# Kernel tuning notes

Hardware: AMD Instinct MI355X
Metric: run time of the kernel (lower is better)

The kernel has to match this reference:

```python
import jax, jax.numpy as jnp
import numpy as np

IOU_TH = 0.5      # iou_threshold
SCORE_TH = 0.5    # confidence_threshold (passed as score_threshold to tf NMS)
MAX_DET = 512     # max_detections


def setup_inputs() -> dict:
    key = jax.random.key(0)
    k1, k2, k3 = jax.random.split(key, 3)
    B, N, C = 8, 2048, 80
    # tf.image.non_max_suppression interprets box columns as corners
    # (y1, x1, y2, x2); generate valid corner boxes in [0, 1].
    mins = jax.random.uniform(k1, (B, N, 2), dtype=jnp.float32)
    sizes = jax.random.uniform(k2, (B, N, 2), dtype=jnp.float32) * 0.2 + 0.01
    box_prediction = jnp.concatenate([mins, mins + sizes], axis=-1)  # [B,N,4]
    class_prediction = jax.random.normal(k3, (B, N, C), dtype=jnp.float32) * 2.0
    return {"box_prediction": box_prediction, "class_prediction": class_prediction}


def _nms_single(boxes, cls_pred, conf):
    """Greedy NMS for one image. boxes [N,4], cls_pred [N,C], conf [N].
    Matches tf.image.non_max_suppression semantics (corner-coordinate IoU,
    score threshold, greedy suppression in descending score order),
    then gathers boxes/cls/conf at the kept indices, padded to MAX_DET."""
    N = boxes.shape[0]
    order = jnp.argsort(-conf)                 # descending scores
    b = boxes[order]                            # [N,4]
    c = cls_pred[order]                         # [N,C]
    s = conf[order]                             # [N]

    bb = jax.lax.stop_gradient(b)               # IoU/indices are non-diff
    y1, x1, y2, x2 = bb[:, 0], bb[:, 1], bb[:, 2], bb[:, 3]
    area = (y2 - y1) * (x2 - x1)                # [N]
    ih = jnp.clip(jnp.minimum(y2[:, None], y2[None, :]) -
                  jnp.maximum(y1[:, None], y1[None, :]), 0.0)
    iw = jnp.clip(jnp.minimum(x2[:, None], x2[None, :]) -
                  jnp.maximum(x1[:, None], x1[None, :]), 0.0)
    inter = ih * iw                             # [N,N]
    union = area[:, None] + area[None, :] - inter
    iou = inter / jnp.maximum(union, 1e-9)      # [N,N]

    valid = s > SCORE_TH                        # score_threshold filter
    idxs = jnp.arange(N)

    def step(keep, xs):
        row, i = xs
        # if box i survives, suppress all later boxes overlapping > IOU_TH
        sup = (row > IOU_TH) & (idxs > i) & keep[i]
        return keep & ~sup, None

    keep, _ = jax.lax.scan(step, valid, (iou, idxs))

    # select kept boxes (already sorted by score) padded to MAX_DET
    masked = jnp.where(keep, s, -1.0)
    top_s, top_idx = jax.lax.top_k(jax.lax.stop_gradient(masked), MAX_DET)
    vm = top_s > SCORE_TH                       # validity of each output slot
    out_box = b[top_idx] * vm[:, None].astype(b.dtype)
    out_cls = c[top_idx] * vm[:, None].astype(c.dtype)
    out_conf = jnp.where(vm, s[top_idx], 0.0)
    return out_box, out_cls, out_conf


def reference(box_prediction, class_prediction):
    # from_logits=True branch of the layer
    class_confidence = jnp.max(jax.nn.sigmoid(class_prediction), axis=-1)  # [B,N]
    cls_prob = jax.nn.softmax(class_prediction, axis=-1)                   # [B,N,C]
    nms_box, nms_cls, nms_conf = jax.vmap(_nms_single)(
        box_prediction, cls_prob, class_confidence)
    return nms_box, nms_cls, nms_conf
```

## Files before the change

### kernel.cpp

```cpp
#include <hip/hip_runtime.h>
#include <stdint.h>

#define BB 8
#define NN 2048
#define NC 80
#define MAXDET 512
#define WPR 32


#define ORD_HALF 0xBF000000u

__global__ __launch_bounds__(64) void k_conf(const float* __restrict__ cls,
                                             uint64_t* __restrict__ keys) {
    int gid = blockIdx.x * 64 + threadIdx.x;
    const float4* p = (const float4*)(cls + (size_t)gid * NC);
    float m = -3.0e38f;
#pragma unroll
    for (int i = 0; i < NC / 4; ++i) {
        float4 v = p[i];
        m = fmaxf(m, fmaxf(fmaxf(v.x, v.y), fmaxf(v.z, v.w)));
    }
    float e  = expf(-m);
    float cf = 1.0f / (1.0f + e);
    uint32_t u = __float_as_uint(cf);
    u = (u & 0x80000000u) ? ~u : (u | 0x80000000u);
    int n = gid & (NN - 1);
    keys[gid] = ((uint64_t)u << 32) | (uint32_t)(NN - 1 - n);
}

#define RCHUNK 128
__global__ __launch_bounds__(512) void k_rank(const uint64_t* __restrict__ keys_in,
                                              uint64_t* __restrict__ keys_out,
                                              const float* __restrict__ boxes,
                                              float* __restrict__ sboxes) {
    __shared__ uint64_t sk[NN];
    __shared__ uint16_t part[4][RCHUNK];
    int b = blockIdx.y, t = threadIdx.x;
    const uint64_t* kin = keys_in + (size_t)b * NN;
#pragma unroll
    for (int j = 0; j < NN / 512; ++j)
        sk[t + j * 512] = kin[t + j * 512];
    __syncthreads();
    int sub = t >> 7;
    int el  = t & (RCHUNK - 1);
    int e   = blockIdx.x * RCHUNK + el;
    uint64_t mykey = sk[e];
    int base = sub * (NN / 4);
    int r = 0;
    for (int mm = 0; mm < NN / 4; ++mm)
        r += (sk[base + mm] > mykey) ? 1 : 0;
    part[sub][el] = (uint16_t)r;
    __syncthreads();
    if (t < RCHUNK) {
        int rank = part[0][t] + part[1][t] + part[2][t] + part[3][t];
        keys_out[(size_t)b * NN + rank] = mykey;
        int orig = (NN - 1) - (int)(mykey & 0xFFFFFFFFull);
        ((float4*)sboxes)[(size_t)b * NN + rank] =
            ((const float4*)boxes)[(size_t)b * NN + orig];
    }
}

__global__ void k_sup(const float* __restrict__ sboxes, uint64_t* __restrict__ sup) {
#pragma clang fp contract(off)
    __shared__ float cy1[256], cx1[256], cy2[256], cx2[256], car[256];
    __shared__ float ry1[64], rx1[64], ry2[64], rx2[64], rar[64];
    int rt = blockIdx.x, ct = blockIdx.y, b = blockIdx.z;
    int t = threadIdx.x;
    int col0 = ct << 8, row0 = rt << 6;
    {
        float4 bx = ((const float4*)sboxes)[(size_t)b * NN + col0 + t];
        cy1[t] = bx.x; cx1[t] = bx.y; cy2[t] = bx.z; cx2[t] = bx.w;
        car[t] = (bx.z - bx.x) * (bx.w - bx.y);
        if (t < 64) {
            float4 rb = ((const float4*)sboxes)[(size_t)b * NN + row0 + t];
            ry1[t] = rb.x; rx1[t] = rb.y; ry2[t] = rb.z; rx2[t] = rb.w;
            rar[t] = (rb.z - rb.x) * (rb.w - rb.y);
        }
    }
    __syncthreads();
    int lr = t & 63, lg = t >> 6;
    int r = row0 + lr;
    int gw = (ct << 2) + lg;
    int cbase = gw << 6;
    uint64_t w = 0;
    if (cbase + 63 > r) {
        float y1 = ry1[lr], x1 = rx1[lr], y2 = ry2[lr], x2 = rx2[lr], ar = rar[lr];
        int lcb = lg << 6;
        for (int c = 0; c < 64; ++c) {
            int lc = lcb + c;
            float ih = fmaxf(fminf(y2, cy2[lc]) - fmaxf(y1, cy1[lc]), 0.0f);
            float iw = fmaxf(fminf(x2, cx2[lc]) - fmaxf(x1, cx1[lc]), 0.0f);
            float inter = ih * iw;
            float uni = (ar + car[lc]) - inter;
            float iou = inter / fmaxf(uni, 1e-9f);
            if ((iou > 0.5f) & ((cbase + c) > r)) w |= (1ull << c);
        }
    }
    sup[((size_t)b * NN + r) * WPR + gw] = w;
}

#define NMS_THREADS 320
__global__ __launch_bounds__(NMS_THREADS) void k_nms(const uint64_t* __restrict__ keys,
                                                     const float* __restrict__ sboxes,
                                                     const uint64_t* __restrict__ sup,
                                                     int* __restrict__ kidx,
                                                     int* __restrict__ kcount,
                                                     float* __restrict__ out_box,
                                                     float* __restrict__ out_conf) {
    __shared__ uint64_t buf[2][64 * WPR];
    __shared__ uint64_t dgT[2][64];
    __shared__ uint8_t  val[NN];
    __shared__ uint64_t kmaskS[WPR];
    __shared__ int pfx[WPR];
    __shared__ int s_kc;
    __shared__ int s_done;
    int b = blockIdx.x, t = threadIdx.x;
    const uint64_t* supb = sup + (size_t)b * NN * WPR;
    const uint64_t* keyb = keys + (size_t)b * NN;

    for (int i = t; i < NN; i += NMS_THREADS)
        val[i] = (uint8_t)((uint32_t)(keyb[i] >> 32) > ORD_HALF);
    if (t < WPR) kmaskS[t] = 0;
    if (t == 0) s_done = 0;
    for (int e = t; e < 64 * WPR / 2; e += NMS_THREADS) {
        ulonglong2 v = ((const ulonglong2*)supb)[e];
        ((ulonglong2*)buf[0])[e] = v;
        if ((e & 15) == 0) dgT[0][e >> 4] = v.x;
    }
    __syncthreads();

    int wave = t >> 6;
    uint64_t kb = 0;
    int cnt = 0;
    if (t < 32) {
        uint64_t vm = 0;
#pragma unroll
        for (int c = 0; c < 64; ++c)
            vm |= ((uint64_t)val[(t << 6) | c]) << c;
        kb = ~vm;
    }
    int l2 = t & 31, half = (t >> 5) & 1;

    for (int g = 0; g < WPR; ++g) {
        if (wave > 0) {
            if (g + 1 < WPR) {
                const ulonglong2* src = (const ulonglong2*)(supb + (size_t)(g + 1) * 64 * WPR);
                ulonglong2* dst = (ulonglong2*)buf[(g + 1) & 1];
                int idx = t - 64;
                ulonglong2 r0 = src[idx];
                ulonglong2 r1 = src[idx + 256];
                ulonglong2 r2 = src[idx + 512];
                ulonglong2 r3 = src[idx + 768];
                dst[idx]       = r0;
                dst[idx + 256] = r1;
                dst[idx + 512] = r2;
                dst[idx + 768] = r3;
                if ((idx & 15) == ((g + 1) >> 1)) {
                    int r = idx >> 4;
                    int hi = (g + 1) & 1;
                    uint64_t* dT = dgT[(g + 1) & 1];
                    dT[r]      = hi ? r0.y : r0.x;
                    dT[r + 16] = hi ? r1.y : r1.x;
                    dT[r + 32] = hi ? r2.y : r2.x;
                    dT[r + 48] = hi ? r3.y : r3.x;
                }
            }
        } else {
            const uint64_t* bufc = buf[g & 1];
            uint64_t diag = dgT[g & 1][t];
            uint32_t dlo = (uint32_t)diag, dhi = (uint32_t)(diag >> 32);
            uint64_t rwv = __shfl(kb, g);
            uint32_t rw_lo = __builtin_amdgcn_readfirstlane((uint32_t)rwv);
            uint32_t rw_hi = __builtin_amdgcn_readfirstlane((uint32_t)(rwv >> 32));
            uint32_t gm_lo = 0, gm_hi = 0;
#pragma unroll
            for (int c = 0; c < 32; ++c) {
                uint32_t rlo = __builtin_amdgcn_readlane(dlo, c);
                uint32_t rhi = __builtin_amdgcn_readlane(dhi, c);
                uint32_t keep = (~(rw_lo >> c)) & 1u;
                uint32_t msk  = 0u - keep;
                rw_lo |= rlo & msk;
                rw_hi |= rhi & msk;
                gm_lo |= keep << c;
            }
#pragma unroll
            for (int c = 0; c < 32; ++c) {
                uint32_t rlo = __builtin_amdgcn_readlane(dlo, c + 32);
                uint32_t rhi = __builtin_amdgcn_readlane(dhi, c + 32);
                uint32_t keep = (~(rw_hi >> c)) & 1u;
                uint32_t msk  = 0u - keep;
                rw_lo |= rlo & msk;
                rw_hi |= rhi & msk;
                gm_hi |= keep << c;
            }
            uint64_t gm = ((uint64_t)gm_hi << 32) | gm_lo;
            uint32_t gmh = half ? gm_hi : gm_lo;
            const uint64_t* rowp = bufc + ((half << 5) * WPR + l2);
            uint64_t acc = 0;
#pragma unroll
            for (int j = 0; j < 32; ++j) {
                uint64_t row = rowp[(size_t)j * WPR];
                acc |= (((gmh >> j) & 1u) ? row : 0ull);
            }
            acc |= __shfl(acc, t ^ 32);
            if (t < 32) kb |= acc;
            if (t == g) kmaskS[g] = gm;
            cnt += __popcll(gm);
            if (cnt >= MAXDET) s_done = 1;
        }
        __syncthreads();
        if (s_done) break;
    }

    if (t == 0) {
        int s = 0;
        for (int w2 = 0; w2 < WPR; ++w2) { pfx[w2] = s; s += __popcll(kmaskS[w2]); }
        s_kc = (s < MAXDET) ? s : MAXDET;
        kcount[b] = s_kc;
    }
    __syncthreads();
    for (int i = t; i < NN; i += NMS_THREADS) {
        uint64_t m = kmaskS[i >> 6];
        if ((m >> (i & 63)) & 1ull) {
            int rank = pfx[i >> 6] + __popcll(m & ((1ull << (i & 63)) - 1ull));
            if (rank < MAXDET) {
                ((float4*)out_box)[(size_t)b * MAXDET + rank] =
                    ((const float4*)sboxes)[(size_t)b * NN + i];
                uint64_t kk = keyb[i];
                uint32_t u = (uint32_t)(kk >> 32);
                float cf = (u & 0x80000000u) ? __uint_as_float(u ^ 0x80000000u)
                                             : __uint_as_float(~u);
                out_conf[(size_t)b * MAXDET + rank] = cf;
                kidx[b * MAXDET + rank] = (NN - 1) - (int)(kk & 0xFFFFFFFFull);
            }
        }
    }
    for (int k = s_kc + t; k < MAXDET; k += NMS_THREADS) {
        ((float4*)out_box)[(size_t)b * MAXDET + k] = make_float4(0.f, 0.f, 0.f, 0.f);
        out_conf[(size_t)b * MAXDET + k] = 0.0f;
    }
}

__global__ void k_softmax(const float* __restrict__ cls, const int* __restrict__ kidx,
                          const int* __restrict__ kcount, float* __restrict__ out_cls) {
    int k = blockIdx.x, b = blockIdx.y, lane = threadIdx.x;
    float* dst = out_cls + ((size_t)b * MAXDET + k) * NC;
    if (k >= kcount[b]) {
        dst[lane] = 0.0f;
        if (lane < NC - 64) dst[64 + lane] = 0.0f;
        return;
    }
    int n = kidx[b * MAXDET + k];
    const float* src = cls + ((size_t)b * NN + n) * NC;
    float x0 = src[lane];
    float x1 = (lane < NC - 64) ? src[64 + lane] : -3.0e38f;
    float m = fmaxf(x0, x1);
    for (int o = 32; o > 0; o >>= 1) m = fmaxf(m, __shfl_xor(m, o));
    float e0 = expf(x0 - m);
    float e1 = (lane < NC - 64) ? expf(x1 - m) : 0.0f;
    float s = e0 + e1;
    for (int o = 32; o > 0; o >>= 1) s += __shfl_xor(s, o);
    dst[lane] = e0 / s;
    if (lane < NC - 64) dst[64 + lane] = e1 / s;
}

extern "C" void kernel_launch(void* const* d_in, const int* in_sizes, int n_in,
                              void* d_out, int out_size, void* d_ws, size_t ws_size,
                              hipStream_t stream) {
    const float* boxes = (const float*)d_in[0];
    const float* cls   = (const float*)d_in[1];
    float* out      = (float*)d_out;
    float* out_box  = out;
    float* out_cls  = out + BB * MAXDET * 4;
    float* out_conf = out + BB * MAXDET * (4 + NC);

    char* ws = (char*)d_ws;
    uint64_t* keysA  = (uint64_t*)(ws + 0);
    uint64_t* keysB  = (uint64_t*)(ws + 131072);
    float*    sboxes = (float*)(ws + 262144);
    int*      kidx   = (int*)(ws + 524288);
    int*      kcount = (int*)(ws + 540672);
    uint64_t* sup    = (uint64_t*)(ws + 544768);

    k_conf<<<(BB * NN) / 64, 64, 0, stream>>>(cls, keysA);
    k_rank<<<dim3(NN / RCHUNK, BB), 512, 0, stream>>>(keysA, keysB, boxes, sboxes);
    k_sup<<<dim3(NN / 64, NN / 256, BB), 256, 0, stream>>>(sboxes, sup);
    k_nms<<<BB, NMS_THREADS, 0, stream>>>(keysB, sboxes, sup, kidx, kcount, out_box, out_conf);
    k_softmax<<<dim3(MAXDET, BB), 64, 0, stream>>>(cls, kidx, kcount, out_cls);
}
```

Before: 80.19 us.

## Prefetch suppression rows two groups ahead with register staging and triple buffer

The NMS kernel's loader waves now issue global loads for group g+2 into registers, while the registers already holding group g+1 are written into a triple-buffered shared array. This hides global-load latency behind a whole iteration instead of stalling on it before the LDS store each step. The cost is extra LDS (a third 16KB buffer plus diagonal slot) and more live registers in the loader waves.

```diff
diff --git a/kernel.cpp b/kernel.cpp
--- a/kernel.cpp
+++ b/kernel.cpp
@@ -107,8 +107,8 @@
                                                      int* __restrict__ kcount,
                                                      float* __restrict__ out_box,
                                                      float* __restrict__ out_conf) {
-    __shared__ uint64_t buf[2][64 * WPR];
-    __shared__ uint64_t dgT[2][64];
+    __shared__ uint64_t buf[3][64 * WPR];
+    __shared__ uint64_t dgT[3][64];
     __shared__ uint8_t  val[NN];
     __shared__ uint64_t kmaskS[WPR];
     __shared__ int pfx[WPR];
@@ -127,9 +127,16 @@
         ((ulonglong2*)buf[0])[e] = v;
         if ((e & 15) == 0) dgT[0][e >> 4] = v.x;
     }
-    __syncthreads();
 
     int wave = t >> 6;
+    int idx = t - 64;
+    ulonglong2 s0 = {}, s1 = {}, s2 = {}, s3 = {};
+    if (wave > 0) {
+        const ulonglong2* src = (const ulonglong2*)(supb + (size_t)64 * WPR);
+        s0 = src[idx]; s1 = src[idx + 256]; s2 = src[idx + 512]; s3 = src[idx + 768];
+    }
+    __syncthreads();
+
     uint64_t kb = 0;
     int cnt = 0;
     if (t < 32) {
@@ -141,33 +148,33 @@
     }
     int l2 = t & 31, half = (t >> 5) & 1;
 
+    int rd = 0;
     for (int g = 0; g < WPR; ++g) {
+        int wr = (rd == 2) ? 0 : rd + 1;
         if (wave > 0) {
             if (g + 1 < WPR) {
-                const ulonglong2* src = (const ulonglong2*)(supb + (size_t)(g + 1) * 64 * WPR);
-                ulonglong2* dst = (ulonglong2*)buf[(g + 1) & 1];
-                int idx = t - 64;
-                ulonglong2 r0 = src[idx];
-                ulonglong2 r1 = src[idx + 256];
-                ulonglong2 r2 = src[idx + 512];
-                ulonglong2 r3 = src[idx + 768];
-                dst[idx]       = r0;
-                dst[idx + 256] = r1;
-                dst[idx + 512] = r2;
-                dst[idx + 768] = r3;
+                ulonglong2* dst = (ulonglong2*)buf[wr];
+                dst[idx]       = s0;
+                dst[idx + 256] = s1;
+                dst[idx + 512] = s2;
+                dst[idx + 768] = s3;
                 if ((idx & 15) == ((g + 1) >> 1)) {
                     int r = idx >> 4;
                     int hi = (g + 1) & 1;
-                    uint64_t* dT = dgT[(g + 1) & 1];
-                    dT[r]      = hi ? r0.y : r0.x;
-                    dT[r + 16] = hi ? r1.y : r1.x;
-                    dT[r + 32] = hi ? r2.y : r2.x;
-                    dT[r + 48] = hi ? r3.y : r3.x;
+                    uint64_t* dT = dgT[wr];
+                    dT[r]      = hi ? s0.y : s0.x;
+                    dT[r + 16] = hi ? s1.y : s1.x;
+                    dT[r + 32] = hi ? s2.y : s2.x;
+                    dT[r + 48] = hi ? s3.y : s3.x;
                 }
             }
+            if (g + 2 < WPR) {
+                const ulonglong2* src = (const ulonglong2*)(supb + (size_t)(g + 2) * 64 * WPR);
+                s0 = src[idx]; s1 = src[idx + 256]; s2 = src[idx + 512]; s3 = src[idx + 768];
+            }
         } else {
-            const uint64_t* bufc = buf[g & 1];
-            uint64_t diag = dgT[g & 1][t];
+            const uint64_t* bufc = buf[rd];
+            uint64_t diag = dgT[rd][t];
             uint32_t dlo = (uint32_t)diag, dhi = (uint32_t)(diag >> 32);
             uint64_t rwv = __shfl(kb, g);
             uint32_t rw_lo = __builtin_amdgcn_readfirstlane((uint32_t)rwv);
@@ -210,6 +217,7 @@
         }
         __syncthreads();
         if (s_done) break;
+        rd = wr;
     }
 
     if (t == 0) {
```

Measured after the change: 80.67 us. No clear change (+0.6%).
